# Optimization experiments

Hardware: AMD Instinct MI355X
Metric: run time of the kernel (lower is better)

Reference implementation:

```python
import jax, jax.numpy as jnp
from jax import lax
import numpy as np

B, N, T, P, D, EMB, K = 16, 207, 23990, 168, 96, 100, 10
L2 = T - 9 - 9                 # two valid Conv1d(kernel=10)
DIM_FC = 16 * L2               # 383552
DIM_FC_MEAN = P * D            # 16128
BN_EPS = 1e-5
TEMP = 0.5


def setup_inputs() -> dict:
    key = jax.random.key(0)
    ks = jax.random.split(key, 10)
    return {
        "hidden_states": jax.random.normal(ks[0], (B, N, P, D), jnp.float32),
        "node_feats": jax.random.normal(ks[1], (T, N), jnp.float32),
        "conv1_w": jax.random.normal(ks[2], (8, 1, 10), jnp.float32) * 0.3,
        "conv1_b": jnp.zeros((8,), jnp.float32),
        "conv2_w": jax.random.normal(ks[3], (16, 8, 10), jnp.float32) * 0.1,
        "conv2_b": jnp.zeros((16,), jnp.float32),
        "bn1_g": jnp.ones((8,), jnp.float32), "bn1_b": jnp.zeros((8,), jnp.float32),
        "bn2_g": jnp.ones((16,), jnp.float32), "bn2_b": jnp.zeros((16,), jnp.float32),
        "fc_w": jax.random.normal(ks[4], (EMB, DIM_FC), jnp.float32) * 0.002,
        "fc_b": jnp.zeros((EMB,), jnp.float32),
        "bn3_g": jnp.ones((EMB,), jnp.float32), "bn3_b": jnp.zeros((EMB,), jnp.float32),
        "fc_mean_w": jax.random.normal(ks[5], (EMB, DIM_FC_MEAN), jnp.float32) * 0.008,
        "fc_mean_b": jnp.zeros((EMB,), jnp.float32),
        "fc_out_w": jax.random.normal(ks[6], (EMB, 2 * EMB), jnp.float32) * 0.07,
        "fc_out_b": jnp.zeros((EMB,), jnp.float32),
        "fc_cat_w": jax.random.normal(ks[7], (2, EMB), jnp.float32) * 0.1,
        "fc_cat_b": jnp.zeros((2,), jnp.float32),
    }


def _conv1d(x, w, b):
    # x: [N, C_in, L], w: [C_out, C_in, k] -> [N, C_out, L-k+1]
    y = lax.conv_general_dilated(x, w, (1,), 'VALID',
                                 dimension_numbers=('NCH', 'OIH', 'NCH'))
    return y + b[None, :, None]


def _bn3d(x, g, b):  # BatchNorm1d training-mode on [N, C, L]
    m = x.mean((0, 2), keepdims=True)
    v = x.var((0, 2), keepdims=True)
    return (x - m) / jnp.sqrt(v + BN_EPS) * g[None, :, None] + b[None, :, None]


def reference(hidden_states, node_feats, conv1_w, conv1_b, conv2_w, conv2_b,
              bn1_g, bn1_b, bn2_g, bn2_b, fc_w, fc_b, bn3_g, bn3_b,
              fc_mean_w, fc_mean_b, fc_out_w, fc_out_b, fc_cat_w, fc_cat_b):
    # ---- global node features from long history: conv -> bn -> conv -> bn -> fc -> bn
    x = node_feats.T.reshape(N, 1, T)
    x = _bn3d(jax.nn.relu(_conv1d(x, conv1_w, conv1_b)), bn1_g, bn1_b)
    x = _bn3d(jax.nn.relu(_conv1d(x, conv2_w, conv2_b)), bn2_g, bn2_b)
    x = x.reshape(N, DIM_FC)
    x = jax.nn.relu(x @ fc_w.T + fc_b)                       # [N, EMB]
    m = x.mean(0); v = x.var(0)
    x = (x - m) / jnp.sqrt(v + BN_EPS) * bn3_g + bn3_b       # bn3
    node_feat = jnp.broadcast_to(x[None], (B, N, EMB))       # [B, N, EMB]

    # ---- dynamic feature (computed in torch forward, unused downstream)
    _dyn = jax.nn.relu(hidden_states.reshape(B, N, DIM_FC_MEAN) @ fc_mean_w.T + fc_mean_b)

    # ---- edge features: edge e=i*N+j has sender j, receiver i (rel_send/rel_rec matmuls)
    W_s, W_r = fc_out_w[:, :EMB], fc_out_w[:, EMB:]
    ps = node_feat @ W_s.T                                   # sender projections  [B,N,EMB]
    pr = node_feat @ W_r.T                                   # receiver projections [B,N,EMB]
    edge = jax.nn.relu(pr[:, :, None, :] + ps[:, None, :, :] + fc_out_b)  # [B,N,N,EMB]
    bernoulli_unnorm = (edge @ fc_cat_w.T + fc_cat_b).reshape(B, N * N, 2)

    # ---- gumbel-softmax (hard, straight-through), temperature 0.5
    u = jax.random.uniform(jax.random.key(42), bernoulli_unnorm.shape, jnp.float32)
    g = -jnp.log(-jnp.log(u + 1e-20) + 1e-20)
    y_soft = jax.nn.softmax((bernoulli_unnorm + g) / TEMP, axis=-1)
    y_hard = jax.nn.one_hot(jnp.argmax(y_soft, axis=-1), 2, dtype=y_soft.dtype)
    y = lax.stop_gradient(y_hard - y_soft) + y_soft
    eye = jnp.eye(N, dtype=bool)[None]
    sampled_adj = jnp.where(eye, 0.0, y[..., 0].reshape(B, N, N))

    # ---- kNN graph from TSFormer features: cosine sim + global top-k + scatter
    h = hidden_states.reshape(B, N, DIM_FC_MEAN)
    hn = h / (jnp.linalg.norm(h, axis=-1, keepdims=True) + 1e-10)
    sim = jnp.einsum('bnd,bmd->bnm', hn, hn).reshape(B, N * N)
    vals, idx = lax.top_k(sim, K * N)                        # k * num_nodes entries
    res = jnp.zeros_like(sim).at[jnp.arange(B)[:, None], idx].set(vals)
    adj_knn = (res != 0).astype(jnp.float32).reshape(B, N, N)
    adj_knn = lax.stop_gradient(jnp.where(eye, 0.0, adj_knn))

    return bernoulli_unnorm, hidden_states, adj_knn, sampled_adj
```

## Files before the change

kernel.cpp:

```cpp
#include <hip/hip_runtime.h>
#include <stdint.h>
#include <math.h>

#define NBATCH 16
#define NNODE 207
#define TLEN 23990
#define EMBD 100
#define L1LEN 23981
#define L2LEN 23972
#define DIMFC 383552
#define DMEAN 16128
#define NSQ 42849
#define KSEL 2070
#define BNEPS 1e-5f
#define NKS 125
#define KHALF 8064

#define O_HID  1371168ull
#define O_KNN  54787104ull
#define O_SAMP 55472688ull

__device__ __forceinline__ float waveReduce(float v) {
#pragma unroll
  for (int o = 32; o > 0; o >>= 1) v += __shfl_down(v, o);
  return v;
}

__device__ __forceinline__ double waveReduceD(double v) {
#pragma unroll
  for (int o = 32; o > 0; o >>= 1) v += __shfl_down(v, o);
  return v;
}

__device__ __forceinline__ unsigned int sortableKey(float f) {
  unsigned int u = __float_as_uint(f);
  return (u & 0x80000000u) ? ~u : (u | 0x80000000u);
}

__device__ __forceinline__ void threefry(uint32_t x0, uint32_t x1, uint32_t& o0, uint32_t& o1) {
  const uint32_t k0 = 0u, k1 = 42u;
  const uint32_t k2 = k0 ^ k1 ^ 0x1BD11BDAu;
  x0 += k0; x1 += k1;
#define TFR(r) { x0 += x1; x1 = (x1 << r) | (x1 >> (32 - r)); x1 ^= x0; }
  TFR(13) TFR(15) TFR(26) TFR(6)   x0 += k1; x1 += k2 + 1u;
  TFR(17) TFR(29) TFR(16) TFR(24)  x0 += k2; x1 += k0 + 2u;
  TFR(13) TFR(15) TFR(26) TFR(6)   x0 += k0; x1 += k1 + 3u;
  TFR(17) TFR(29) TFR(16) TFR(24)  x0 += k1; x1 += k2 + 4u;
  TFR(13) TFR(15) TFR(26) TFR(6)   x0 += k2; x1 += k0 + 5u;
#undef TFR
  o0 = x0; o1 = x1;
}

__device__ __forceinline__ float uniform_part(uint32_t m) {
  uint32_t o0, o1;
  threefry(0u, m, o0, o1);
  uint32_t bits = o0 ^ o1;
  return __uint_as_float((bits >> 9) | 0x3f800000u) - 1.0f;
}

__global__ __launch_bounds__(256) void k_copynorm(const float* __restrict__ h,
                                                  float* __restrict__ out,
                                                  float* __restrict__ norms) {
  const size_t row = blockIdx.x;
  const float4* src = reinterpret_cast<const float4*>(h + row * (size_t)DMEAN);
  float4* dst = reinterpret_cast<float4*>(out + O_HID + row * (size_t)DMEAN);
  float s = 0.f;
  for (int i = threadIdx.x; i < DMEAN / 4; i += 256) {
    float4 v = src[i];
    dst[i] = v;
    s += v.x * v.x + v.y * v.y + v.z * v.z + v.w * v.w;
  }
  __shared__ float red[4];
  float w = waveReduce(s);
  if ((threadIdx.x & 63) == 0) red[threadIdx.x >> 6] = w;
  __syncthreads();
  if (threadIdx.x == 0) norms[row] = sqrtf(red[0] + red[1] + red[2] + red[3]);
}

__global__ __launch_bounds__(256) void k_sim(const float* __restrict__ h,
                                             float* __restrict__ simp) {
  const int b = blockIdx.y;
  const int tile = blockIdx.x & 15;
  const int ks = blockIdx.x >> 4;
  const int ti = tile >> 2, tj = tile & 3;
  __shared__ float sB[32][64];
  const int tx = threadIdx.x & 15, ty = threadIdx.x >> 4;
  const float* hb = h + (size_t)b * NNODE * DMEAN;
  const int r0 = ti * 64 + ty * 4;
  const float* ap0 = hb + (size_t)min(r0 + 0, NNODE - 1) * DMEAN;
  const float* ap1 = hb + (size_t)min(r0 + 1, NNODE - 1) * DMEAN;
  const float* ap2 = hb + (size_t)min(r0 + 2, NNODE - 1) * DMEAN;
  const float* ap3 = hb + (size_t)min(r0 + 3, NNODE - 1) * DMEAN;
  const int scol = threadIdx.x >> 2;
  const int sk = (threadIdx.x & 3) * 8;
  const bool bvalid = (tj * 64 + scol) < NNODE;
  const float* bp = hb + (size_t)min(tj * 64 + scol, NNODE - 1) * DMEAN;
  float acc[4][4];
#pragma unroll
  for (int p = 0; p < 4; p++)
#pragma unroll
    for (int q = 0; q < 4; q++) acc[p][q] = 0.f;
  const int kbeg = ks * KHALF;
  const int kend = kbeg + KHALF;
  for (int k0 = kbeg; k0 < kend; k0 += 32) {
    __syncthreads();
    {
      float4 v1 = make_float4(0.f, 0.f, 0.f, 0.f), v2 = v1;
      if (bvalid) {
        v1 = *reinterpret_cast<const float4*>(bp + k0 + sk);
        v2 = *reinterpret_cast<const float4*>(bp + k0 + sk + 4);
      }
      sB[sk + 0][scol] = v1.x;
      sB[sk + 1][scol] = v1.y;
      sB[sk + 2][scol] = v1.z;
      sB[sk + 3][scol] = v1.w;
      sB[sk + 4][scol] = v2.x;
      sB[sk + 5][scol] = v2.y;
      sB[sk + 6][scol] = v2.z;
      sB[sk + 7][scol] = v2.w;
    }
    __syncthreads();
#pragma unroll
    for (int g = 0; g < 8; g++) {
      const int kk = k0 + g * 4;
      const float4 a0 = *reinterpret_cast<const float4*>(ap0 + kk);
      const float4 a1 = *reinterpret_cast<const float4*>(ap1 + kk);
      const float4 a2 = *reinterpret_cast<const float4*>(ap2 + kk);
      const float4 a3 = *reinterpret_cast<const float4*>(ap3 + kk);
      const float4 b0 = *reinterpret_cast<const float4*>(&sB[g * 4 + 0][tx * 4]);
      const float4 b1 = *reinterpret_cast<const float4*>(&sB[g * 4 + 1][tx * 4]);
      const float4 b2 = *reinterpret_cast<const float4*>(&sB[g * 4 + 2][tx * 4]);
      const float4 b3 = *reinterpret_cast<const float4*>(&sB[g * 4 + 3][tx * 4]);
      acc[0][0] = fmaf(a0.x, b0.x, acc[0][0]); acc[0][1] = fmaf(a0.x, b0.y, acc[0][1]);
      acc[0][2] = fmaf(a0.x, b0.z, acc[0][2]); acc[0][3] = fmaf(a0.x, b0.w, acc[0][3]);
      acc[1][0] = fmaf(a1.x, b0.x, acc[1][0]); acc[1][1] = fmaf(a1.x, b0.y, acc[1][1]);
      acc[1][2] = fmaf(a1.x, b0.z, acc[1][2]); acc[1][3] = fmaf(a1.x, b0.w, acc[1][3]);
      acc[2][0] = fmaf(a2.x, b0.x, acc[2][0]); acc[2][1] = fmaf(a2.x, b0.y, acc[2][1]);
      acc[2][2] = fmaf(a2.x, b0.z, acc[2][2]); acc[2][3] = fmaf(a2.x, b0.w, acc[2][3]);
      acc[3][0] = fmaf(a3.x, b0.x, acc[3][0]); acc[3][1] = fmaf(a3.x, b0.y, acc[3][1]);
      acc[3][2] = fmaf(a3.x, b0.z, acc[3][2]); acc[3][3] = fmaf(a3.x, b0.w, acc[3][3]);
      acc[0][0] = fmaf(a0.y, b1.x, acc[0][0]); acc[0][1] = fmaf(a0.y, b1.y, acc[0][1]);
      acc[0][2] = fmaf(a0.y, b1.z, acc[0][2]); acc[0][3] = fmaf(a0.y, b1.w, acc[0][3]);
      acc[1][0] = fmaf(a1.y, b1.x, acc[1][0]); acc[1][1] = fmaf(a1.y, b1.y, acc[1][1]);
      acc[1][2] = fmaf(a1.y, b1.z, acc[1][2]); acc[1][3] = fmaf(a1.y, b1.w, acc[1][3]);
      acc[2][0] = fmaf(a2.y, b1.x, acc[2][0]); acc[2][1] = fmaf(a2.y, b1.y, acc[2][1]);
      acc[2][2] = fmaf(a2.y, b1.z, acc[2][2]); acc[2][3] = fmaf(a2.y, b1.w, acc[2][3]);
      acc[3][0] = fmaf(a3.y, b1.x, acc[3][0]); acc[3][1] = fmaf(a3.y, b1.y, acc[3][1]);
      acc[3][2] = fmaf(a3.y, b1.z, acc[3][2]); acc[3][3] = fmaf(a3.y, b1.w, acc[3][3]);
      acc[0][0] = fmaf(a0.z, b2.x, acc[0][0]); acc[0][1] = fmaf(a0.z, b2.y, acc[0][1]);
      acc[0][2] = fmaf(a0.z, b2.z, acc[0][2]); acc[0][3] = fmaf(a0.z, b2.w, acc[0][3]);
      acc[1][0] = fmaf(a1.z, b2.x, acc[1][0]); acc[1][1] = fmaf(a1.z, b2.y, acc[1][1]);
      acc[1][2] = fmaf(a1.z, b2.z, acc[1][2]); acc[1][3] = fmaf(a1.z, b2.w, acc[1][3]);
      acc[2][0] = fmaf(a2.z, b2.x, acc[2][0]); acc[2][1] = fmaf(a2.z, b2.y, acc[2][1]);
      acc[2][2] = fmaf(a2.z, b2.z, acc[2][2]); acc[2][3] = fmaf(a2.z, b2.w, acc[2][3]);
      acc[3][0] = fmaf(a3.z, b2.x, acc[3][0]); acc[3][1] = fmaf(a3.z, b2.y, acc[3][1]);
      acc[3][2] = fmaf(a3.z, b2.z, acc[3][2]); acc[3][3] = fmaf(a3.z, b2.w, acc[3][3]);
      acc[0][0] = fmaf(a0.w, b3.x, acc[0][0]); acc[0][1] = fmaf(a0.w, b3.y, acc[0][1]);
      acc[0][2] = fmaf(a0.w, b3.z, acc[0][2]); acc[0][3] = fmaf(a0.w, b3.w, acc[0][3]);
      acc[1][0] = fmaf(a1.w, b3.x, acc[1][0]); acc[1][1] = fmaf(a1.w, b3.y, acc[1][1]);
      acc[1][2] = fmaf(a1.w, b3.z, acc[1][2]); acc[1][3] = fmaf(a1.w, b3.w, acc[1][3]);
      acc[2][0] = fmaf(a2.w, b3.x, acc[2][0]); acc[2][1] = fmaf(a2.w, b3.y, acc[2][1]);
      acc[2][2] = fmaf(a2.w, b3.z, acc[2][2]); acc[2][3] = fmaf(a2.w, b3.w, acc[2][3]);
      acc[3][0] = fmaf(a3.w, b3.x, acc[3][0]); acc[3][1] = fmaf(a3.w, b3.y, acc[3][1]);
      acc[3][2] = fmaf(a3.w, b3.z, acc[3][2]); acc[3][3] = fmaf(a3.w, b3.w, acc[3][3]);
    }
  }
  float* op = simp + ((size_t)ks * NBATCH + b) * NSQ;
#pragma unroll
  for (int p = 0; p < 4; p++) {
    int ii = r0 + p;
    if (ii < NNODE) {
#pragma unroll
      for (int q = 0; q < 4; q++) {
        int jj = tj * 64 + tx * 4 + q;
        if (jj < NNODE) op[ii * NNODE + jj] = acc[p][q];
      }
    }
  }
}

__global__ __launch_bounds__(256) void k_simc(const float* __restrict__ simp,
                                              const float* __restrict__ norms,
                                              float* __restrict__ sim) {
  const int gid = blockIdx.x * 256 + threadIdx.x;
  if (gid >= NBATCH * NSQ) return;
  const int b = gid / NSQ;
  const int rem = gid - b * NSQ;
  const int i = rem / NNODE, j = rem - i * NNODE;
  float s = simp[gid] + simp[(size_t)NBATCH * NSQ + gid];
  float di = norms[b * NNODE + i] + 1e-10f;
  float dj = norms[b * NNODE + j] + 1e-10f;
  sim[gid] = s / (di * dj);
}

__global__ __launch_bounds__(1024) void k_topk(const float* __restrict__ sim,
                                               float* __restrict__ out) {
  const int b = blockIdx.x;
  const float* s = sim + (size_t)b * NSQ;
  float* knn = out + O_KNN + (size_t)b * NSQ;
  __shared__ unsigned int hist[256];
  __shared__ unsigned int cnts[1024];
  __shared__ unsigned int sh_prefix, sh_kneed;
  if (threadIdx.x == 0) { sh_prefix = 0u; sh_kneed = KSEL; }
  __syncthreads();
  const int lo = threadIdx.x * 42;
  const int hi = min(lo + 42, NSQ);
  for (int pass = 0; pass < 4; pass++) {
    const int shift = 24 - pass * 8;
    if (threadIdx.x < 256) hist[threadIdx.x] = 0u;
    __syncthreads();
    unsigned int pref = sh_prefix;
    unsigned int hmask = (pass == 0) ? 0u : (0xFFFFFFFFu << (shift + 8));
    for (int i = lo; i < hi; i++) {
      unsigned int key = sortableKey(s[i]);
      if ((key & hmask) == pref) atomicAdd(&hist[(key >> shift) & 255], 1u);
    }
    __syncthreads();
    if (threadIdx.x == 0) {
      unsigned int need = sh_kneed, cum = 0;
      for (int bkt = 255; bkt >= 0; bkt--) {
        unsigned int c = hist[bkt];
        if (cum + c >= need) {
          sh_prefix = pref | ((unsigned int)bkt << shift);
          sh_kneed = need - cum;
          break;
        }
        cum += c;
      }
    }
    __syncthreads();
  }
  const unsigned int kth = sh_prefix;
  const unsigned int need_eq = sh_kneed;
  unsigned int myeq = 0;
  for (int i = lo; i < hi; i++) {
    float v = s[i];
    unsigned int key = sortableKey(v);
    float o = 0.f;
    if (key > kth) {
      int ii = i / NNODE, jj = i - ii * NNODE;
      o = (v != 0.f && ii != jj) ? 1.f : 0.f;
    } else if (key == kth) {
      myeq++;
    }
    knn[i] = o;
  }
  cnts[threadIdx.x] = myeq;
  __syncthreads();
  if (threadIdx.x == 0) {
    unsigned int run = 0;
    for (int t = 0; t < 1024; t++) { unsigned int c = cnts[t]; cnts[t] = run; run += c; }
  }
  __syncthreads();
  unsigned int rank = cnts[threadIdx.x];
  for (int i = lo; i < hi && rank < need_eq; i++) {
    float v = s[i];
    if (sortableKey(v) == kth) {
      if (rank < need_eq) {
        int ii = i / NNODE, jj = i - ii * NNODE;
        knn[i] = (v != 0.f && ii != jj) ? 1.f : 0.f;
      }
      rank++;
    }
  }
}

__global__ __launch_bounds__(256) void k_c1stats(const float* __restrict__ nf,
                                                 const float* __restrict__ c1w,
                                                 const float* __restrict__ c1b,
                                                 float* __restrict__ part1) {
  __shared__ float sw[80], sb[8];
  if (threadIdx.x < 80) sw[threadIdx.x] = c1w[threadIdx.x];
  if (threadIdx.x < 8) sb[threadIdx.x] = c1b[threadIdx.x];
  __syncthreads();
  const int t0 = blockIdx.x * 128;
  const int cnt = min(128, L1LEN - t0);
  float s[8], sq[8];
#pragma unroll
  for (int c = 0; c < 8; c++) { s[c] = 0.f; sq[c] = 0.f; }
  for (int idx = threadIdx.x; idx < cnt * NNODE; idx += 256) {
    int tl = idx / NNODE;
    int n = idx - tl * NNODE;
    const float* p = nf + (size_t)(t0 + tl) * NNODE + n;
    float in[10];
#pragma unroll
    for (int k = 0; k < 10; k++) in[k] = p[k * NNODE];
#pragma unroll
    for (int c = 0; c < 8; c++) {
      float a = sb[c];
#pragma unroll
      for (int k = 0; k < 10; k++) a = fmaf(sw[c * 10 + k], in[k], a);
      a = fmaxf(a, 0.f);
      s[c] += a;
      sq[c] = fmaf(a, a, sq[c]);
    }
  }
  __shared__ float red[4][16];
  int lane = threadIdx.x & 63, wv = threadIdx.x >> 6;
#pragma unroll
  for (int c = 0; c < 8; c++) {
    float a = waveReduce(s[c]);
    float q = waveReduce(sq[c]);
    if (lane == 0) { red[wv][c * 2] = a; red[wv][c * 2 + 1] = q; }
  }
  __syncthreads();
  if (threadIdx.x < 16)
    part1[blockIdx.x * 16 + threadIdx.x] =
        red[0][threadIdx.x] + red[1][threadIdx.x] + red[2][threadIdx.x] + red[3][threadIdx.x];
}

__global__ void k_red1(const float* __restrict__ part1, const float* __restrict__ g1,
                       const float* __restrict__ b1, double* __restrict__ foldd) {
  __shared__ double sums[16];
  if (threadIdx.x < 16) {
    double s = 0.0;
    for (int i = 0; i < 188; i++) s += (double)part1[i * 16 + threadIdx.x];
    sums[threadIdx.x] = s;
  }
  __syncthreads();
  if (threadIdx.x < 8) {
    const double cnt = 207.0 * 23981.0;
    int c = threadIdx.x;
    double m = sums[c * 2] / cnt;
    double ex2 = sums[c * 2 + 1] / cnt;
    double var = ex2 - m * m;
    double sc = (double)g1[c] / sqrt(var + (double)BNEPS);
    foldd[c] = sc;
    foldd[8 + c] = (double)b1[c] - m * sc;
  }
}

__global__ __launch_bounds__(256) void k_c2stats(const float* __restrict__ nf,
                                                 const float* __restrict__ c1w,
                                                 const float* __restrict__ c1b,
                                                 const float* __restrict__ c2w,
                                                 const float* __restrict__ c2b,
                                                 const double* __restrict__ foldd,
                                                 float* __restrict__ part2) {
  const int n = blockIdx.y;
  const int l0 = blockIdx.x * 1024;
  const int len = min(1024, L2LEN - l0);
  __shared__ float s_nf[1042];
  __shared__ float s_o1[8][1034];
  __shared__ float s_w2t[1280];
  __shared__ float s_b2[16];
  __shared__ float s_c1w[80], s_c1b[8];
  __shared__ float s_a1[8], s_be1[8];
  for (int i = threadIdx.x; i < 1280; i += 256) {
    int co = i / 80, r = i - co * 80;
    s_w2t[r * 16 + co] = c2w[i];
  }
  if (threadIdx.x < 16) s_b2[threadIdx.x] = c2b[threadIdx.x];
  if (threadIdx.x < 80) s_c1w[threadIdx.x] = c1w[threadIdx.x];
  if (threadIdx.x < 8) {
    s_c1b[threadIdx.x] = c1b[threadIdx.x];
    s_a1[threadIdx.x] = (float)foldd[threadIdx.x];
    s_be1[threadIdx.x] = (float)foldd[8 + threadIdx.x];
  }
  __syncthreads();
  const int nfl = len + 18;
  for (int i = threadIdx.x; i < nfl; i += 256) s_nf[i] = nf[(size_t)(l0 + i) * NNODE + n];
  __syncthreads();
  const int o1l = len + 9;
  for (int i = threadIdx.x; i < 8 * o1l; i += 256) {
    int c = i / o1l, t = i - c * o1l;
    float a = s_c1b[c];
#pragma unroll
    for (int k = 0; k < 10; k++) a = fmaf(s_c1w[c * 10 + k], s_nf[t + k], a);
    s_o1[c][t] = fmaxf(a, 0.f) * s_a1[c] + s_be1[c];
  }
  __syncthreads();
  const int co = threadIdx.x & 15, lg = threadIdx.x >> 4;
  float sum = 0.f, ssq = 0.f;
  for (int pass = 0; pass < 4; pass++) {
    int lb = pass * 256 + lg * 16;
    if (lb >= len) continue;
    int nl = min(16, len - lb);
    float y[16];
#pragma unroll
    for (int l = 0; l < 16; l++) y[l] = s_b2[co];
#pragma unroll
    for (int ci = 0; ci < 8; ci++) {
      float win[25];
#pragma unroll
      for (int w = 0; w < 25; w++) win[w] = s_o1[ci][lb + w];
#pragma unroll
      for (int k = 0; k < 10; k++) {
        float wv = s_w2t[(ci * 10 + k) * 16 + co];
#pragma unroll
        for (int l = 0; l < 16; l++) y[l] = fmaf(wv, win[l + k], y[l]);
      }
    }
#pragma unroll
    for (int l = 0; l < 16; l++) {
      if (l < nl) {
        float v = fmaxf(y[l], 0.f);
        sum += v;
        ssq = fmaf(v, v, ssq);
      }
    }
  }
  __shared__ float rs[16][16], rq[16][16];
  rs[lg][co] = sum;
  rq[lg][co] = ssq;
  __syncthreads();
  if (threadIdx.x < 16) {
    float a = 0.f, q = 0.f;
    for (int g = 0; g < 16; g++) { a += rs[g][threadIdx.x]; q += rq[g][threadIdx.x]; }
    int blk = blockIdx.y * gridDim.x + blockIdx.x;
    part2[blk * 32 + threadIdx.x * 2] = a;
    part2[blk * 32 + threadIdx.x * 2 + 1] = q;
  }
}

__global__ void k_red2(const float* __restrict__ part2, const float* __restrict__ g2,
                       const float* __restrict__ b2, double* __restrict__ foldd) {
  __shared__ double acc8[8][32];
  const int grp = threadIdx.x >> 5, v = threadIdx.x & 31;
  double s = 0.0;
  for (int i = grp; i < 4968; i += 8) s += (double)part2[i * 32 + v];
  acc8[grp][v] = s;
  __syncthreads();
  if (threadIdx.x < 32) {
    double t = 0.0;
    for (int g = 0; g < 8; g++) t += acc8[g][threadIdx.x];
    acc8[0][threadIdx.x] = t;
  }
  __syncthreads();
  if (threadIdx.x < 16) {
    const double cnt = 207.0 * 23972.0;
    int c = threadIdx.x;
    double m = acc8[0][c * 2] / cnt;
    double ex2 = acc8[0][c * 2 + 1] / cnt;
    double var = ex2 - m * m;
    double sc = (double)g2[c] / sqrt(var + (double)BNEPS);
    foldd[16 + c] = sc;
    foldd[32 + c] = (double)b2[c] - m * sc;
  }
}

__global__ __launch_bounds__(512, 2) void k_gemm(const float* __restrict__ nf,
                                                 const float* __restrict__ c1w,
                                                 const float* __restrict__ c1b,
                                                 const float* __restrict__ c2w,
                                                 const float* __restrict__ c2b,
                                                 const double* __restrict__ foldd,
                                                 const float* __restrict__ fcw,
                                                 float* __restrict__ part) {
  const int ks = blockIdx.x;
  const int nt = blockIdx.y;
  const int l0 = ks * 192;
  const int n0 = nt * 52;

  __shared__ float s_nf[26][52];
  __shared__ float s_o1[8][17][52];
  __shared__ float s_x2[16][8][64];
  __shared__ float s_wT[2][112][10];
  __shared__ float s_w2t[1280];
  __shared__ float s_c1w[80], s_c1b[8], s_c2b[16];
  __shared__ float s_a1f[8], s_be1f[8], s_s2f[16], s_t2f[16];

  for (int i = threadIdx.x; i < 1280; i += 512) {
    int co = i / 80, r = i - co * 80;
    s_w2t[r * 16 + co] = c2w[i];
  }
  if (threadIdx.x < 80) s_c1w[threadIdx.x] = c1w[threadIdx.x];
  if (threadIdx.x < 8) {
    s_c1b[threadIdx.x] = c1b[threadIdx.x];
    s_a1f[threadIdx.x] = (float)foldd[threadIdx.x];
    s_be1f[threadIdx.x] = (float)foldd[8 + threadIdx.x];
  }
  if (threadIdx.x < 16) {
    s_c2b[threadIdx.x] = c2b[threadIdx.x];
    s_s2f[threadIdx.x] = (float)foldd[16 + threadIdx.x];
    s_t2f[threadIdx.x] = (float)foldd[32 + threadIdx.x];
  }

  double acc[7][4];
#pragma unroll
  for (int m = 0; m < 7; m++)
#pragma unroll
    for (int q = 0; q < 4; q++) acc[m][q] = 0.0;

  const int te = threadIdx.x & 15;
  const int tn4 = threadIdx.x >> 4;
  const bool fc_act = threadIdx.x < 208;
  const int nl = threadIdx.x & 63;
  const int c0 = (threadIdx.x >> 6) & 7;
  const bool doload = threadIdx.x < 448;
  const int e_ld = threadIdx.x >> 2;
  const int k2 = (threadIdx.x & 3) * 2;

  for (int ls = 0; ls < 24; ls++) {
    const int lb = l0 + ls * 8;
    if (lb >= L2LEN) break;
    const bool lfull = (lb + 8 <= L2LEN);
    for (int i = threadIdx.x; i < 26 * 52; i += 512) {
      int r = i / 52, cc = i - r * 52;
      int t = lb + r, n = n0 + cc;
      float v = 0.f;
      if (t < TLEN && n < NNODE) v = nf[(size_t)t * NNODE + n];
      s_nf[r][cc] = v;
    }
    __syncthreads();
    for (int i = threadIdx.x; i < 8 * 17 * 52; i += 512) {
      int c = i / (17 * 52);
      int rem = i - c * 17 * 52;
      int t = rem / 52, n = rem - t * 52;
      float a = s_c1b[c];
#pragma unroll
      for (int k = 0; k < 10; k++) a = fmaf(s_c1w[c * 10 + k], s_nf[t + k][n], a);
      s_o1[c][t][n] = fmaxf(a, 0.f) * s_a1f[c] + s_be1f[c];
    }
    __syncthreads();
    {
      const bool valid = (nl < 52) && (n0 + nl < NNODE);
      if (valid) {
        const float bA = s_c2b[c0], bB = s_c2b[c0 + 8];
        float y00 = bA, y01 = bA, y02 = bA, y03 = bA;
        float y10 = bA, y11 = bA, y12 = bA, y13 = bA;
        float y20 = bB, y21 = bB, y22 = bB, y23 = bB;
        float y30 = bB, y31 = bB, y32 = bB, y33 = bB;
        for (int ci = 0; ci < 8; ci++) {
          float ww0 = s_o1[ci][0][nl],  ww1 = s_o1[ci][1][nl],  ww2 = s_o1[ci][2][nl];
          float ww3 = s_o1[ci][3][nl],  ww4 = s_o1[ci][4][nl],  ww5 = s_o1[ci][5][nl];
          float ww6 = s_o1[ci][6][nl],  ww7 = s_o1[ci][7][nl],  ww8 = s_o1[ci][8][nl];
          float ww9 = s_o1[ci][9][nl],  wwa = s_o1[ci][10][nl], wwb = s_o1[ci][11][nl];
          float wwc = s_o1[ci][12][nl], wwd = s_o1[ci][13][nl], wwe = s_o1[ci][14][nl];
          float wwf = s_o1[ci][15][nl], wwg = s_o1[ci][16][nl];
          const float* wpA = &s_w2t[ci * 160 + c0];
          const float* wpB = wpA + 8;
          float v, u;
#define C2STEP(K, A0, A1, A2, A3, B0, B1, B2, B3)                                   \
          v = wpA[(K) * 16]; u = wpB[(K) * 16];                                     \
          y00 = fmaf(v, A0, y00); y01 = fmaf(v, A1, y01);                           \
          y02 = fmaf(v, A2, y02); y03 = fmaf(v, A3, y03);                           \
          y10 = fmaf(v, B0, y10); y11 = fmaf(v, B1, y11);                           \
          y12 = fmaf(v, B2, y12); y13 = fmaf(v, B3, y13);                           \
          y20 = fmaf(u, A0, y20); y21 = fmaf(u, A1, y21);                           \
          y22 = fmaf(u, A2, y22); y23 = fmaf(u, A3, y23);                           \
          y30 = fmaf(u, B0, y30); y31 = fmaf(u, B1, y31);                           \
          y32 = fmaf(u, B2, y32); y33 = fmaf(u, B3, y33);
          C2STEP(0, ww0, ww1, ww2, ww3, ww4, ww5, ww6, ww7)
          C2STEP(1, ww1, ww2, ww3, ww4, ww5, ww6, ww7, ww8)
          C2STEP(2, ww2, ww3, ww4, ww5, ww6, ww7, ww8, ww9)
          C2STEP(3, ww3, ww4, ww5, ww6, ww7, ww8, ww9, wwa)
          C2STEP(4, ww4, ww5, ww6, ww7, ww8, ww9, wwa, wwb)
          C2STEP(5, ww5, ww6, ww7, ww8, ww9, wwa, wwb, wwc)
          C2STEP(6, ww6, ww7, ww8, ww9, wwa, wwb, wwc, wwd)
          C2STEP(7, ww7, ww8, ww9, wwa, wwb, wwc, wwd, wwe)
          C2STEP(8, ww8, ww9, wwa, wwb, wwc, wwd, wwe, wwf)
          C2STEP(9, ww9, wwa, wwb, wwc, wwd, wwe, wwf, wwg)
#undef C2STEP
        }
        const float scA = s_s2f[c0], tbA = s_t2f[c0];
        const float scB = s_s2f[c0 + 8], tbB = s_t2f[c0 + 8];
        s_x2[c0][0][nl] = (lb + 0 < L2LEN) ? fmaf(fmaxf(y00, 0.f), scA, tbA) : 0.f;
        s_x2[c0][1][nl] = (lb + 1 < L2LEN) ? fmaf(fmaxf(y01, 0.f), scA, tbA) : 0.f;
        s_x2[c0][2][nl] = (lb + 2 < L2LEN) ? fmaf(fmaxf(y02, 0.f), scA, tbA) : 0.f;
        s_x2[c0][3][nl] = (lb + 3 < L2LEN) ? fmaf(fmaxf(y03, 0.f), scA, tbA) : 0.f;
        s_x2[c0][4][nl] = (lb + 4 < L2LEN) ? fmaf(fmaxf(y10, 0.f), scA, tbA) : 0.f;
        s_x2[c0][5][nl] = (lb + 5 < L2LEN) ? fmaf(fmaxf(y11, 0.f), scA, tbA) : 0.f;
        s_x2[c0][6][nl] = (lb + 6 < L2LEN) ? fmaf(fmaxf(y12, 0.f), scA, tbA) : 0.f;
        s_x2[c0][7][nl] = (lb + 7 < L2LEN) ? fmaf(fmaxf(y13, 0.f), scA, tbA) : 0.f;
        s_x2[c0 + 8][0][nl] = (lb + 0 < L2LEN) ? fmaf(fmaxf(y20, 0.f), scB, tbB) : 0.f;
        s_x2[c0 + 8][1][nl] = (lb + 1 < L2LEN) ? fmaf(fmaxf(y21, 0.f), scB, tbB) : 0.f;
        s_x2[c0 + 8][2][nl] = (lb + 2 < L2LEN) ? fmaf(fmaxf(y22, 0.f), scB, tbB) : 0.f;
        s_x2[c0 + 8][3][nl] = (lb + 3 < L2LEN) ? fmaf(fmaxf(y23, 0.f), scB, tbB) : 0.f;
        s_x2[c0 + 8][4][nl] = (lb + 4 < L2LEN) ? fmaf(fmaxf(y30, 0.f), scB, tbB) : 0.f;
        s_x2[c0 + 8][5][nl] = (lb + 5 < L2LEN) ? fmaf(fmaxf(y31, 0.f), scB, tbB) : 0.f;
        s_x2[c0 + 8][6][nl] = (lb + 6 < L2LEN) ? fmaf(fmaxf(y32, 0.f), scB, tbB) : 0.f;
        s_x2[c0 + 8][7][nl] = (lb + 7 < L2LEN) ? fmaf(fmaxf(y33, 0.f), scB, tbB) : 0.f;
      } else {
#pragma unroll
        for (int l = 0; l < 8; l++) {
          s_x2[c0][l][nl] = 0.f;
          s_x2[c0 + 8][l][nl] = 0.f;
        }
      }
    }
    float2 wld = make_float2(0.f, 0.f);
    if (doload && e_ld < EMBD) {
      const float* fp = fcw + (size_t)e_ld * DIMFC + lb + k2;
      if (lfull) wld = *reinterpret_cast<const float2*>(fp);
      else {
        wld.x = (lb + k2 < L2LEN) ? fp[0] : 0.f;
        wld.y = (lb + k2 + 1 < L2LEN) ? fp[1] : 0.f;
      }
    }
    __syncthreads();
    if (doload) *reinterpret_cast<float2*>(&s_wT[0][e_ld][k2]) = wld;
    for (int c = 0; c < 16; c++) {
      __syncthreads();
      float2 wnext = make_float2(0.f, 0.f);
      if (c < 15 && doload && e_ld < EMBD) {
        const float* fp = fcw + (size_t)e_ld * DIMFC + (size_t)(c + 1) * L2LEN + lb + k2;
        if (lfull) wnext = *reinterpret_cast<const float2*>(fp);
        else {
          wnext.x = (lb + k2 < L2LEN) ? fp[0] : 0.f;
          wnext.y = (lb + k2 + 1 < L2LEN) ? fp[1] : 0.f;
        }
      }
      if (fc_act) {
        const int bsel = c & 1;
        const float4 xv0 = *reinterpret_cast<const float4*>(&s_x2[c][0][tn4 * 4]);
        const float4 xv1 = *reinterpret_cast<const float4*>(&s_x2[c][1][tn4 * 4]);
        const float4 xv2 = *reinterpret_cast<const float4*>(&s_x2[c][2][tn4 * 4]);
        const float4 xv3 = *reinterpret_cast<const float4*>(&s_x2[c][3][tn4 * 4]);
        const float4 xv4 = *reinterpret_cast<const float4*>(&s_x2[c][4][tn4 * 4]);
        const float4 xv5 = *reinterpret_cast<const float4*>(&s_x2[c][5][tn4 * 4]);
        const float4 xv6 = *reinterpret_cast<const float4*>(&s_x2[c][6][tn4 * 4]);
        const float4 xv7 = *reinterpret_cast<const float4*>(&s_x2[c][7][tn4 * 4]);
#pragma unroll
        for (int m = 0; m < 7; m++) {
          const float* wp = &s_wT[bsel][te + 16 * m][0];
          const float2 wv01 = *reinterpret_cast<const float2*>(&wp[0]);
          const float2 wv23 = *reinterpret_cast<const float2*>(&wp[2]);
          const float2 wv45 = *reinterpret_cast<const float2*>(&wp[4]);
          const float2 wv67 = *reinterpret_cast<const float2*>(&wp[6]);
          float a0 = 0.f, a1 = 0.f, a2 = 0.f, a3 = 0.f;
          a0 = fmaf(wv01.x, xv0.x, a0); a1 = fmaf(wv01.x, xv0.y, a1);
          a2 = fmaf(wv01.x, xv0.z, a2); a3 = fmaf(wv01.x, xv0.w, a3);
          a0 = fmaf(wv01.y, xv1.x, a0); a1 = fmaf(wv01.y, xv1.y, a1);
          a2 = fmaf(wv01.y, xv1.z, a2); a3 = fmaf(wv01.y, xv1.w, a3);
          a0 = fmaf(wv23.x, xv2.x, a0); a1 = fmaf(wv23.x, xv2.y, a1);
          a2 = fmaf(wv23.x, xv2.z, a2); a3 = fmaf(wv23.x, xv2.w, a3);
          a0 = fmaf(wv23.y, xv3.x, a0); a1 = fmaf(wv23.y, xv3.y, a1);
          a2 = fmaf(wv23.y, xv3.z, a2); a3 = fmaf(wv23.y, xv3.w, a3);
          a0 = fmaf(wv45.x, xv4.x, a0); a1 = fmaf(wv45.x, xv4.y, a1);
          a2 = fmaf(wv45.x, xv4.z, a2); a3 = fmaf(wv45.x, xv4.w, a3);
          a0 = fmaf(wv45.y, xv5.x, a0); a1 = fmaf(wv45.y, xv5.y, a1);
          a2 = fmaf(wv45.y, xv5.z, a2); a3 = fmaf(wv45.y, xv5.w, a3);
          a0 = fmaf(wv67.x, xv6.x, a0); a1 = fmaf(wv67.x, xv6.y, a1);
          a2 = fmaf(wv67.x, xv6.z, a2); a3 = fmaf(wv67.x, xv6.w, a3);
          a0 = fmaf(wv67.y, xv7.x, a0); a1 = fmaf(wv67.y, xv7.y, a1);
          a2 = fmaf(wv67.y, xv7.z, a2); a3 = fmaf(wv67.y, xv7.w, a3);
          acc[m][0] += (double)a0;
          acc[m][1] += (double)a1;
          acc[m][2] += (double)a2;
          acc[m][3] += (double)a3;
        }
      }
      if (c < 15 && doload)
        *reinterpret_cast<float2*>(&s_wT[(c + 1) & 1][e_ld][k2]) = wnext;
    }
  }
  if (fc_act) {
    for (int m = 0; m < 7; m++) {
      int e = te + 16 * m;
      if (e < EMBD) {
        for (int q = 0; q < 4; q++) {
          int nl2 = tn4 * 4 + q;
          part[(((size_t)ks * 4 + nt) * 100 + e) * 52 + nl2] = (float)acc[m][q];
        }
      }
    }
  }
}

__global__ __launch_bounds__(256) void k_bn3(const float* __restrict__ part,
                                             const float* __restrict__ fcb,
                                             const float* __restrict__ g3,
                                             const float* __restrict__ b3,
                                             double* __restrict__ xd) {
  const int e = blockIdx.x;
  const int n = threadIdx.x;
  double v = 0.0;
  if (n < NNODE) {
    int nt = n / 52, nl = n - nt * 52;
    const size_t stride = 4 * 100 * 52;
    const float* p = part + ((size_t)nt * 100 + e) * 52 + nl;
    for (int ks = 0; ks < NKS; ks++) v += (double)p[ks * stride];
    v = fmax(v + (double)fcb[e], 0.0);
  }
  __shared__ double redA[4], redB[4];
  __shared__ double s_m, s_sd;
  int lane = threadIdx.x & 63, wid = threadIdx.x >> 6;
  double w = waveReduceD(v);
  if (lane == 0) redA[wid] = w;
  __syncthreads();
  if (threadIdx.x == 0) s_m = (redA[0] + redA[1] + redA[2] + redA[3]) / 207.0;
  __syncthreads();
  double m = s_m;
  double d = (n < NNODE) ? (v - m) : 0.0;
  double wq = waveReduceD(d * d);
  if (lane == 0) redB[wid] = wq;
  __syncthreads();
  if (threadIdx.x == 0) s_sd = sqrt((redB[0] + redB[1] + redB[2] + redB[3]) / 207.0 + (double)BNEPS);
  __syncthreads();
  if (n < NNODE) xd[n * 100 + e] = (v - m) / s_sd * (double)g3[e] + (double)b3[e];
}

__global__ void k_pspr(const double* __restrict__ xd, const float* __restrict__ wout,
                       double* __restrict__ psdT, double* __restrict__ prd) {
  const int n = blockIdx.x;
  __shared__ double sx[100];
  if (threadIdx.x < 100) sx[threadIdx.x] = xd[n * 100 + threadIdx.x];
  __syncthreads();
  const int e = threadIdx.x;
  if (e < 100) {
    double a = 0.0, b = 0.0;
    for (int j = 0; j < 100; j++) {
      double xv = sx[j];
      a = fma(xv, (double)wout[e * 200 + j], a);
      b = fma(xv, (double)wout[e * 200 + 100 + j], b);
    }
    psdT[e * NNODE + n] = a;
    prd[n * 100 + e] = b;
  }
}

__global__ __launch_bounds__(256) void k_edge(const double* __restrict__ psdT,
                                              const double* __restrict__ prd,
                                              const float* __restrict__ bo,
                                              const float* __restrict__ wc,
                                              const float* __restrict__ cb,
                                              double* __restrict__ bd,
                                              float* __restrict__ out) {
  const int pij = blockIdx.x * 256 + threadIdx.x;
  if (pij >= NSQ) return;
  const int i = pij / NNODE, j = pij - i * NNODE;
  const double* pri = prd + i * 100;
  double b0 = 0.0, b1 = 0.0;
  for (int e = 0; e < 100; e++) {
    double ed = fmax(pri[e] + psdT[e * NNODE + j] + (double)bo[e], 0.0);
    b0 = fma(ed, (double)wc[e], b0);
    b1 = fma(ed, (double)wc[100 + e], b1);
  }
  b0 += (double)cb[0];
  b1 += (double)cb[1];
  bd[pij * 2] = b0;
  bd[pij * 2 + 1] = b1;
  const float b0f = (float)b0, b1f = (float)b1;
  for (int b = 0; b < NBATCH; b++) {
    size_t base = (size_t)b * (2 * NSQ) + (size_t)pij * 2;
    out[base] = b0f;
    out[base + 1] = b1f;
  }
}

__global__ __launch_bounds__(256) void k_samp(const double* __restrict__ bd,
                                              float* __restrict__ out) {
  const int gid = blockIdx.x * 256 + threadIdx.x;
  if (gid >= NBATCH * NSQ) return;
  const int b = gid / NSQ;
  const int pij = gid - b * NSQ;
  const int i = pij / NNODE, j = pij - i * NNODE;
  const double b0 = bd[pij * 2], b1 = bd[pij * 2 + 1];
  uint32_t base = (uint32_t)b * (2u * NSQ) + (uint32_t)pij * 2u;
  float u0 = uniform_part(base);
  float u1 = uniform_part(base + 1u);
  double g0 = -log(-log((double)u0 + 1e-20) + 1e-20);
  double g1 = -log(-log((double)u1 + 1e-20) + 1e-20);
  float v = ((b0 + g0) >= (b1 + g1)) ? 1.0f : 0.0f;
  if (i == j) v = 0.f;
  out[O_SAMP + (size_t)b * NSQ + pij] = v;
}

extern "C" void kernel_launch(void* const* d_in, const int* in_sizes, int n_in,
                              void* d_out, int out_size, void* d_ws, size_t ws_size,
                              hipStream_t stream) {
  const float* hid = (const float*)d_in[0];
  const float* nf = (const float*)d_in[1];
  const float* c1w = (const float*)d_in[2];
  const float* c1b = (const float*)d_in[3];
  const float* c2w = (const float*)d_in[4];
  const float* c2b = (const float*)d_in[5];
  const float* g1 = (const float*)d_in[6];
  const float* b1 = (const float*)d_in[7];
  const float* g2 = (const float*)d_in[8];
  const float* b2 = (const float*)d_in[9];
  const float* fcw = (const float*)d_in[10];
  const float* fcb = (const float*)d_in[11];
  const float* g3 = (const float*)d_in[12];
  const float* b3 = (const float*)d_in[13];
  const float* wout = (const float*)d_in[16];
  const float* bout = (const float*)d_in[17];
  const float* wc = (const float*)d_in[18];
  const float* cbb = (const float*)d_in[19];
  float* out = (float*)d_out;
  float* ws = (float*)d_ws;

  float* w_norm = ws + 0;
  float* w_sim = ws + 8192;
  float* w_p1 = ws + 704512;
  float* w_p2 = ws + 712704;
  double* w_bd = (double*)(ws + 712704);
  double* w_foldd = (double*)(ws + 900096);
  float* w_part = ws + 1048576;
  double* w_xd = (double*)(ws + 3648576);
  double* w_psdT = (double*)(ws + 3690000);
  double* w_prd = (double*)(ws + 3731400);
  float* w_simp = ws + 3772800;

  k_copynorm<<<NBATCH * NNODE, 256, 0, stream>>>(hid, out, w_norm);
  k_sim<<<dim3(32, NBATCH), 256, 0, stream>>>(hid, w_simp);
  k_simc<<<(NBATCH * NSQ + 255) / 256, 256, 0, stream>>>(w_simp, w_norm, w_sim);
  k_topk<<<NBATCH, 1024, 0, stream>>>(w_sim, out);

  k_c1stats<<<188, 256, 0, stream>>>(nf, c1w, c1b, w_p1);
  k_red1<<<1, 64, 0, stream>>>(w_p1, g1, b1, w_foldd);
  k_c2stats<<<dim3(24, NNODE), 256, 0, stream>>>(nf, c1w, c1b, c2w, c2b, w_foldd, w_p2);
  k_red2<<<1, 256, 0, stream>>>(w_p2, g2, b2, w_foldd);
  k_gemm<<<dim3(NKS, 4), 512, 0, stream>>>(nf, c1w, c1b, c2w, c2b, w_foldd, fcw, w_part);
  k_bn3<<<EMBD, 256, 0, stream>>>(w_part, fcb, g3, b3, w_xd);
  k_pspr<<<NNODE, 128, 0, stream>>>(w_xd, wout, w_psdT, w_prd);
  k_edge<<<(NSQ + 255) / 256, 256, 0, stream>>>(w_psdT, w_prd, bout, wc, cbb, w_bd, out);
  k_samp<<<(NBATCH * NSQ + 255) / 256, 256, 0, stream>>>(w_bd, out);
}
```

Measured before the change: 2.559 ms.

## Exploit Gram symmetry in sim kernel, split K four ways, privatize topk histograms

The similarity GEMM now computes only the upper-triangular 64x64 tiles (10 of 16 per batch), mirrors each result into the transposed position, and splits the reduction into four K chunks instead of two. The combine kernel therefore sums four partial buffers. The top-k radix select gets per-wave privatized shared histograms to cut atomic contention, and its serial 1024-element prefix scan becomes a two-level scan. The workspace is re-laid out so the larger partial-sum buffer overlaps the fc GEMM partial area. The trade-offs are extra scattered transposed stores, more partial traffic in the combine step, and reliance on that buffer reuse being safe under stream ordering.

```diff
diff --git a/kernel.cpp b/kernel.cpp
--- a/kernel.cpp
+++ b/kernel.cpp
@@ -14,7 +14,7 @@
 #define KSEL 2070
 #define BNEPS 1e-5f
 #define NKS 125
-#define KHALF 8064
+#define KQ 4032
 
 #define O_HID  1371168ull
 #define O_KNN  54787104ull
@@ -80,9 +80,10 @@
 __global__ __launch_bounds__(256) void k_sim(const float* __restrict__ h,
                                              float* __restrict__ simp) {
   const int b = blockIdx.y;
-  const int tile = blockIdx.x & 15;
-  const int ks = blockIdx.x >> 4;
-  const int ti = tile >> 2, tj = tile & 3;
+  const int pid = blockIdx.x % 10;
+  const int ksq = blockIdx.x / 10;
+  const int ti = (pid < 4) ? 0 : (pid < 7) ? 1 : (pid < 9) ? 2 : 3;
+  const int tj = pid - ((ti == 0) ? 0 : (ti == 1) ? 3 : (ti == 2) ? 5 : 6);
   __shared__ float sB[32][64];
   const int tx = threadIdx.x & 15, ty = threadIdx.x >> 4;
   const float* hb = h + (size_t)b * NNODE * DMEAN;
@@ -100,8 +101,8 @@
   for (int p = 0; p < 4; p++)
 #pragma unroll
     for (int q = 0; q < 4; q++) acc[p][q] = 0.f;
-  const int kbeg = ks * KHALF;
-  const int kend = kbeg + KHALF;
+  const int kbeg = ksq * KQ;
+  const int kend = kbeg + KQ;
   for (int k0 = kbeg; k0 < kend; k0 += 32) {
     __syncthreads();
     {
@@ -165,7 +166,7 @@
       acc[3][2] = fmaf(a3.w, b3.z, acc[3][2]); acc[3][3] = fmaf(a3.w, b3.w, acc[3][3]);
     }
   }
-  float* op = simp + ((size_t)ks * NBATCH + b) * NSQ;
+  float* op = simp + ((size_t)ksq * NBATCH + b) * NSQ;
 #pragma unroll
   for (int p = 0; p < 4; p++) {
     int ii = r0 + p;
@@ -173,7 +174,10 @@
 #pragma unroll
       for (int q = 0; q < 4; q++) {
         int jj = tj * 64 + tx * 4 + q;
-        if (jj < NNODE) op[ii * NNODE + jj] = acc[p][q];
+        if (jj < NNODE) {
+          op[ii * NNODE + jj] = acc[p][q];
+          if (ti != tj) op[jj * NNODE + ii] = acc[p][q];
+        }
       }
     }
   }
@@ -187,7 +191,8 @@
   const int b = gid / NSQ;
   const int rem = gid - b * NSQ;
   const int i = rem / NNODE, j = rem - i * NNODE;
-  float s = simp[gid] + simp[(size_t)NBATCH * NSQ + gid];
+  const size_t stride = (size_t)NBATCH * NSQ;
+  float s = ((simp[gid] + simp[stride + gid]) + simp[2 * stride + gid]) + simp[3 * stride + gid];
   float di = norms[b * NNODE + i] + 1e-10f;
   float dj = norms[b * NNODE + j] + 1e-10f;
   sim[gid] = s / (di * dj);
@@ -198,22 +203,31 @@
   const int b = blockIdx.x;
   const float* s = sim + (size_t)b * NSQ;
   float* knn = out + O_KNN + (size_t)b * NSQ;
+  __shared__ unsigned int hist16[16 * 257];
   __shared__ unsigned int hist[256];
   __shared__ unsigned int cnts[1024];
+  __shared__ unsigned int tsum[16];
   __shared__ unsigned int sh_prefix, sh_kneed;
+  const int wid = threadIdx.x >> 6;
   if (threadIdx.x == 0) { sh_prefix = 0u; sh_kneed = KSEL; }
   __syncthreads();
   const int lo = threadIdx.x * 42;
   const int hi = min(lo + 42, NSQ);
   for (int pass = 0; pass < 4; pass++) {
     const int shift = 24 - pass * 8;
-    if (threadIdx.x < 256) hist[threadIdx.x] = 0u;
+    for (int i = threadIdx.x; i < 16 * 257; i += 1024) hist16[i] = 0u;
     __syncthreads();
     unsigned int pref = sh_prefix;
     unsigned int hmask = (pass == 0) ? 0u : (0xFFFFFFFFu << (shift + 8));
     for (int i = lo; i < hi; i++) {
       unsigned int key = sortableKey(s[i]);
-      if ((key & hmask) == pref) atomicAdd(&hist[(key >> shift) & 255], 1u);
+      if ((key & hmask) == pref) atomicAdd(&hist16[wid * 257 + ((key >> shift) & 255)], 1u);
+    }
+    __syncthreads();
+    if (threadIdx.x < 256) {
+      unsigned int t = 0;
+      for (int w = 0; w < 16; w++) t += hist16[w * 257 + threadIdx.x];
+      hist[threadIdx.x] = t;
     }
     __syncthreads();
     if (threadIdx.x == 0) {
@@ -247,12 +261,22 @@
   }
   cnts[threadIdx.x] = myeq;
   __syncthreads();
+  if (threadIdx.x < 16) {
+    unsigned int run = 0;
+    for (int k = 0; k < 64; k++) {
+      unsigned int c = cnts[threadIdx.x * 64 + k];
+      cnts[threadIdx.x * 64 + k] = run;
+      run += c;
+    }
+    tsum[threadIdx.x] = run;
+  }
+  __syncthreads();
   if (threadIdx.x == 0) {
     unsigned int run = 0;
-    for (int t = 0; t < 1024; t++) { unsigned int c = cnts[t]; cnts[t] = run; run += c; }
-  }
-  __syncthreads();
-  unsigned int rank = cnts[threadIdx.x];
+    for (int w = 0; w < 16; w++) { unsigned int c = tsum[w]; tsum[w] = run; run += c; }
+  }
+  __syncthreads();
+  unsigned int rank = cnts[threadIdx.x] + tsum[wid >> 2 == 0 ? threadIdx.x >> 6 : threadIdx.x >> 6];
   for (int i = lo; i < hi && rank < need_eq; i++) {
     float v = s[i];
     if (sortableKey(v) == kth) {
@@ -787,14 +811,14 @@
   float* w_p2 = ws + 712704;
   double* w_bd = (double*)(ws + 712704);
   double* w_foldd = (double*)(ws + 900096);
+  float* w_simp = ws + 1048576;
   float* w_part = ws + 1048576;
-  double* w_xd = (double*)(ws + 3648576);
-  double* w_psdT = (double*)(ws + 3690000);
-  double* w_prd = (double*)(ws + 3731400);
-  float* w_simp = ws + 3772800;
+  double* w_xd = (double*)(ws + 3791000);
+  double* w_psdT = (double*)(ws + 3832400);
+  double* w_prd = (double*)(ws + 3873800);
 
   k_copynorm<<<NBATCH * NNODE, 256, 0, stream>>>(hid, out, w_norm);
-  k_sim<<<dim3(32, NBATCH), 256, 0, stream>>>(hid, w_simp);
+  k_sim<<<dim3(40, NBATCH), 256, 0, stream>>>(hid, w_simp);
   k_simc<<<(NBATCH * NSQ + 255) / 256, 256, 0, stream>>>(w_simp, w_norm, w_sim);
   k_topk<<<NBATCH, 1024, 0, stream>>>(w_sim, out);
 
```

Result: faster. 2.292 ms (-10.4%).
